# Performance work log

Measured on AMD Instinct MI355X. Metric: run time of the kernel, lower is better.

The kernel has to match this reference:

```python
import jax, jax.numpy as jnp
import numpy as np

X_DIM = 20000   # number of input locations (x_l rows)
Y_DIM = 6000    # number of query locations (y_l rows)
REGION_DEG = 10.0  # lon/lat spread so every query has neighbors within 250 km
EARTH_DIAM = 2.0 * 6.378  # thousand-km diameter used by the source
THRESH = 0.25   # 250 km neighborhood threshold


def setup_inputs() -> dict:
    key = jax.random.key(0)
    k1, k2, k3 = jax.random.split(key, 3)
    x = jax.random.normal(k1, (X_DIM, 1), dtype=jnp.float32)
    x_l = jax.random.uniform(k2, (X_DIM, 2), dtype=jnp.float32) * REGION_DEG
    y_l = jax.random.uniform(k3, (Y_DIM, 2), dtype=jnp.float32) * REGION_DEG
    return {"x": x, "x_l": x_l, "y_l": y_l}


def reference(x, x_l, y_l):
    # Training branch of GPR.call, vectorized over the y_dim python loop.
    d2r = jnp.pi / 180.0
    lon_x, lat_x = x_l[:, 0], x_l[:, 1]   # (X,)
    lon_y, lat_y = y_l[:, 0], y_l[:, 1]   # (Y,)
    # haversine terms, shape (Y, X)
    hav = jnp.sin((lat_x[None, :] - lat_y[:, None]) * d2r) ** 2
    hav = hav + (jnp.cos(lat_x * d2r)[None, :] * jnp.cos(lat_y * d2r)[:, None]
                 * jnp.sin((lon_x[None, :] - lon_y[:, None]) * d2r) ** 2)
    d = EARTH_DIAM * jnp.arcsin(jnp.sqrt(hav))  # great-circle distance (thousand km)
    # threshold + gather/scatter in source == masked weights here
    w = jnp.where(d < THRESH, d, 0.0)
    s = jnp.sum(w, axis=1, keepdims=True)        # (Y, 1) per-row normalizer
    L = jnp.where(s > 0, w / jnp.maximum(s, 1e-12), 0.0)  # (Y, X) sparse-ish weights
    m = (L @ x)[:, 0]                            # (Y,) squeezed mean
    # V = 0.001 * I  (noise=None path); returned value is diag_part(V)
    v_diag = jnp.full((y_l.shape[0],), 0.001, dtype=x.dtype)
    return m, v_diag
```

## Files before the change

### kernel.cpp

```cpp
#include <hip/hip_runtime.h>
#include <math.h>


#define TPB    256
#define YPB    4
#define NSTRIP 40
#define NLON   40
#define NCELLS (NSTRIP * NLON)
#define C_CELL   0.25f
#define INV_CELL 4.0f
#define RLAT     1.1250f

__device__ __forceinline__ float sin_poly(float a) {
    float t = a * a;
    return a * fmaf(t, fmaf(t, 8.3333333e-3f, -0.16666667f), 1.0f);
}
__device__ __forceinline__ float cos_poly(float a) {
    float t = a * a;
    return fmaf(t, fmaf(t, fmaf(t, -1.3888889e-3f, 4.1666668e-2f), -0.5f), 1.0f);
}
__device__ __forceinline__ int cell_of(float lon, float lat) {
    int s = (int)(lat * INV_CELL); s = min(max(s, 0), NSTRIP - 1);
    int l = (int)(lon * INV_CELL); l = min(max(l, 0), NLON - 1);
    return s * NLON + l;
}


__global__ __launch_bounds__(TPB) void zero_kernel(int* __restrict__ histX,
                                                   int* __restrict__ histY) {
    for (int i = threadIdx.x; i < NCELLS; i += TPB) { histX[i] = 0; histY[i] = 0; }
}

__global__ __launch_bounds__(TPB) void hist_kernel(
    const float* __restrict__ x_l, const float* __restrict__ y_l,
    int* __restrict__ histX, int* __restrict__ histY, int nx, int ny)
{
    int i = blockIdx.x * TPB + threadIdx.x;
    if (i < nx) {
        atomicAdd(&histX[cell_of(x_l[2 * i], x_l[2 * i + 1])], 1);
    } else if (i < nx + ny) {
        int j = i - nx;
        atomicAdd(&histY[cell_of(y_l[2 * j], y_l[2 * j + 1])], 1);
    }
}

__global__ __launch_bounds__(TPB) void scan_kernel(
    const int* __restrict__ histX, const int* __restrict__ histY,
    int* __restrict__ csX, int* __restrict__ csY,
    int* __restrict__ curX, int* __restrict__ curY)
{
    const int CHUNK = (NCELLS + TPB - 1) / TPB;
    __shared__ int sums[TPB];
    const int* hist      = (blockIdx.x == 0) ? histX : histY;
    int*       cellStart = (blockIdx.x == 0) ? csX  : csY;
    int*       cursor    = (blockIdx.x == 0) ? curX : curY;

    int tid = threadIdx.x;
    int base = tid * CHUNK;
    int local[7];
    int s = 0;
    #pragma unroll
    for (int j = 0; j < CHUNK; ++j) {
        int idx = base + j;
        int v = (idx < NCELLS) ? hist[idx] : 0;
        local[j] = s; s += v;
    }
    sums[tid] = s;
    __syncthreads();
    for (int off = 1; off < TPB; off <<= 1) {
        int t = (tid >= off) ? sums[tid - off] : 0;
        __syncthreads();
        sums[tid] += t;
        __syncthreads();
    }
    int excl = (tid > 0) ? sums[tid - 1] : 0;
    #pragma unroll
    for (int j = 0; j < CHUNK; ++j) {
        int idx = base + j;
        if (idx < NCELLS) { cellStart[idx] = excl + local[j]; cursor[idx] = excl + local[j]; }
    }
    if (tid == TPB - 1) cellStart[NCELLS] = sums[TPB - 1];
}

__global__ __launch_bounds__(TPB) void scatter_kernel(
    const float* __restrict__ x, const float* __restrict__ x_l,
    const float* __restrict__ y_l,
    int* __restrict__ curX, int* __restrict__ curY,
    float4* __restrict__ sortedA, float2* __restrict__ sortedRaw,
    float*  __restrict__ sortedX,
    float2* __restrict__ sortedYL, int* __restrict__ sortedYIdx,
    int nx, int ny)
{
    const float d2r = 0.017453292519943295f;
    int i = blockIdx.x * TPB + threadIdx.x;
    if (i < nx) {
        float lon = x_l[2 * i], lat = x_l[2 * i + 1];
        int pos = atomicAdd(&curX[cell_of(lon, lat)], 1);
        float al = lat * d2r, ao = lon * d2r;
        sortedA[pos]   = make_float4(sin_poly(al), cos_poly(al),
                                     sin_poly(ao), cos_poly(ao));
        sortedRaw[pos] = make_float2(lon, lat);
        sortedX[pos]   = x[i];
    } else if (i < nx + ny) {
        int j = i - nx;
        float lon = y_l[2 * j], lat = y_l[2 * j + 1];
        int pos = atomicAdd(&curY[cell_of(lon, lat)], 1);
        sortedYL[pos]   = make_float2(lon, lat);
        sortedYIdx[pos] = j;
    }
}


__global__ __launch_bounds__(TPB) void gpr_binned(
    const float4* __restrict__ sortedA,
    const float2* __restrict__ sortedRaw,
    const float*  __restrict__ sortedX,
    const int*    __restrict__ cellStart,
    const float2* __restrict__ sortedYL,
    const int*    __restrict__ sortedYIdx,
    float* __restrict__ out, int ny, float Hcut, float HcutM)
{
    const int tid  = threadIdx.x;
    const int wave = tid >> 6;
    const int lane = tid & 63;
    const int j    = blockIdx.x * YPB + wave;

    const float d2r    = 0.017453292519943295f;
    const float r2d    = 57.29577951308232f;
    const float THRESH = 0.25f;
    const float DIAM   = 12.756f;
    const float DIAM6  = 12.756f / 6.0f;
    const float EPS_H  = 5e-8f;

    int   yidx  = 0;
    float lon_y = 0.0f, lat_y = 0.0f;
    if (j < ny) {
        yidx = sortedYIdx[j];
        float2 p = sortedYL[j];
        lon_y = p.x; lat_y = p.y;
    }
    const float sly   = sin_poly(lat_y * d2r);
    const float cly   = cos_poly(lat_y * d2r);
    const float slony = sin_poly(lon_y * d2r);
    const float clony = cos_poly(lon_y * d2r);

    float accw = 0.0f, accwx = 0.0f;

    const int s0 = max(0,          (int)floorf((lat_y - RLAT) * INV_CELL));
    const int s1 = min(NSTRIP - 1, (int)floorf((lat_y + RLAT) * INV_CELL));

    for (int s = s0; s <= s1; ++s) {
        float slo = s * C_CELL, shi = slo + C_CELL;
        float dmin = fmaxf(0.0f, fmaxf(slo - lat_y, lat_y - shi));
        float de   = fmaxf(0.0f, dmin - 3e-3f);
        float sd_  = sin_poly(de * d2r);
        float rem  = HcutM - sd_ * sd_;
        if (rem <= 0.0f) continue;
        float ccm = cos_poly(fminf(shi, 10.0f) * d2r) * cly * 0.999999f;
        float W   = asinf(fminf(1.0f, sqrtf(rem / ccm))) * r2d + 4e-3f;
        int lo = min(NLON - 1, max(0, (int)floorf((lon_y - W) * INV_CELL)));
        int hi = min(NLON - 1, max(0, (int)floorf((lon_y + W) * INV_CELL)));
        int p0 = cellStart[s * NLON + lo];
        int p1 = cellStart[s * NLON + hi + 1];

        for (int k = p0 + lane; k < p1; k += 64) {
            float4 e  = sortedA[k];
            float  xv = sortedX[k];

            float sl  = fmaf(e.x, cly,   -(e.y * sly));
            float sd  = fmaf(e.z, clony, -(e.w * slony));
            float cxy = e.y * cly;
            float hav = fmaf(sl, sl, cxy * (sd * sd));

            float tb  = hav - Hcut;
            float r   = __builtin_amdgcn_sqrtf(hav);
            float d   = r * fmaf(hav, DIAM6, DIAM);

            float w;
            if (__builtin_expect(fabsf(tb) < EPS_H, 0)) {
                float2 raw = sortedRaw[k];
                float lonx = raw.x, latx = raw.y;

                float dlat = __fsub_rn(latx, lat_y);
                float alat = __fmul_rn(dlat, d2r);
                float slf  = (float)sin((double)alat);
                float h1   = __fmul_rn(slf, slf);

                float axl  = __fmul_rn(latx,  d2r);
                float ayl  = __fmul_rn(lat_y, d2r);
                float cxf  = (float)cos((double)axl);
                float cyf  = (float)cos((double)ayl);
                float cc   = __fmul_rn(cxf, cyf);

                float dlon = __fsub_rn(lonx, lon_y);
                float alon = __fmul_rn(dlon, d2r);
                float sdf  = (float)sin((double)alon);
                float h2   = __fmul_rn(sdf, sdf);

                float hv   = __fadd_rn(h1, __fmul_rn(cc, h2));
                float r32  = (float)sqrt((double)hv);
                float as32 = (float)asin((double)r32);
                float dnp  = __fmul_rn(DIAM, as32);
                w = (dnp < THRESH) ? dnp : 0.0f;
            } else {
                w = (tb < 0.0f) ? d : 0.0f;
            }

            accw += w;
            accwx = fmaf(w, xv, accwx);
        }
    }

    #pragma unroll
    for (int off = 32; off > 0; off >>= 1) {
        accw  += __shfl_xor(accw,  off, 64);
        accwx += __shfl_xor(accwx, off, 64);
    }

    if (lane == 0 && j < ny) {
        float m = (accw > 0.0f) ? (accwx / fmaxf(accw, 1e-12f)) : 0.0f;
        out[yidx]      = m;
        out[ny + yidx] = 0.001f;
    }
}


__global__ __launch_bounds__(TPB) void gpr_full(
    const float* __restrict__ x, const float* __restrict__ x_l,
    const float* __restrict__ y_l, float* __restrict__ out,
    int nx, int ny, float Hcut)
{
    __shared__ float4 tA[1024];
    __shared__ float  tX[1024];

    const int tid  = threadIdx.x;
    const int wave = tid >> 6;
    const int lane = tid & 63;
    const int y    = blockIdx.x * YPB + wave;

    const float d2r    = 0.017453292519943295f;
    const float THRESH = 0.25f;
    const float DIAM   = 12.756f;
    const float DIAM6  = 12.756f / 6.0f;
    const float EPS_H  = 5e-8f;

    float lon_y = 0.0f, lat_y = 0.0f;
    if (y < ny) { lon_y = y_l[2 * y]; lat_y = y_l[2 * y + 1]; }
    const float sly   = sin_poly(lat_y * d2r);
    const float cly   = cos_poly(lat_y * d2r);
    const float slony = sin_poly(lon_y * d2r);
    const float clony = cos_poly(lon_y * d2r);

    float accw = 0.0f, accwx = 0.0f;

    const int ntiles = (nx + 1023) / 1024;
    for (int t = 0; t < ntiles; ++t) {
        const int base = t * 1024;
        __syncthreads();
        #pragma unroll
        for (int jj = 0; jj < 1024 / TPB; ++jj) {
            int idx = jj * TPB + tid, i = base + idx;
            if (i < nx) {
                float lon = x_l[2 * i], lat = x_l[2 * i + 1];
                tA[idx] = make_float4(sin_poly(lat * d2r), cos_poly(lat * d2r),
                                      sin_poly(lon * d2r), cos_poly(lon * d2r));
                tX[idx] = x[i];
            }
        }
        __syncthreads();

        const int tn = min(1024, nx - base);
        for (int k = lane; k < tn; k += 64) {
            float4 e  = tA[k];
            float  xv = tX[k];
            float sl  = fmaf(e.x, cly,   -(e.y * sly));
            float sd  = fmaf(e.z, clony, -(e.w * slony));
            float cxy = e.y * cly;
            float hav = fmaf(sl, sl, cxy * (sd * sd));
            float tb  = hav - Hcut;
            float r   = __builtin_amdgcn_sqrtf(hav);
            float d   = r * fmaf(hav, DIAM6, DIAM);
            float w;
            if (__builtin_expect(fabsf(tb) < EPS_H, 0)) {
                int   i    = base + k;
                float lonx = x_l[2 * i], latx = x_l[2 * i + 1];
                float dlat = __fsub_rn(latx, lat_y);
                float alat = __fmul_rn(dlat, d2r);
                float slf  = (float)sin((double)alat);
                float h1   = __fmul_rn(slf, slf);
                float axl  = __fmul_rn(latx,  d2r);
                float ayl  = __fmul_rn(lat_y, d2r);
                float cxf  = (float)cos((double)axl);
                float cyf  = (float)cos((double)ayl);
                float cc   = __fmul_rn(cxf, cyf);
                float dlon = __fsub_rn(lonx, lon_y);
                float alon = __fmul_rn(dlon, d2r);
                float sdf  = (float)sin((double)alon);
                float h2   = __fmul_rn(sdf, sdf);
                float hv   = __fadd_rn(h1, __fmul_rn(cc, h2));
                float r32  = (float)sqrt((double)hv);
                float as32 = (float)asin((double)r32);
                float dnp  = __fmul_rn(DIAM, as32);
                w = (dnp < THRESH) ? dnp : 0.0f;
            } else {
                w = (tb < 0.0f) ? d : 0.0f;
            }
            accw += w;
            accwx = fmaf(w, xv, accwx);
        }
    }

    #pragma unroll
    for (int off = 32; off > 0; off >>= 1) {
        accw  += __shfl_xor(accw,  off, 64);
        accwx += __shfl_xor(accwx, off, 64);
    }

    if (lane == 0 && y < ny) {
        float m = (accw > 0.0f) ? (accwx / fmaxf(accw, 1e-12f)) : 0.0f;
        out[y]      = m;
        out[ny + y] = 0.001f;
    }
}


extern "C" void kernel_launch(void* const* d_in, const int* in_sizes, int n_in,
                              void* d_out, int out_size, void* d_ws, size_t ws_size,
                              hipStream_t stream) {
    const float* x   = (const float*)d_in[0];
    const float* x_l = (const float*)d_in[1];
    const float* y_l = (const float*)d_in[2];
    float* out = (float*)d_out;

    const int nx = in_sizes[0];
    const int ny = in_sizes[2] / 2;

    double th = 0.25 / 12.756;
    double s  = sin(th);
    float Hcut  = (float)(s * s);
    float HcutM = (float)(s * s * 1.001);

    size_t offA   = 0;
    size_t offRaw = offA   + (size_t)nx * sizeof(float4);
    size_t offYL  = offRaw + (size_t)nx * sizeof(float2);
    size_t offX   = offYL  + (size_t)ny * sizeof(float2);
    size_t offYI  = offX   + (size_t)nx * sizeof(float);
    size_t offHX  = offYI  + (size_t)ny * sizeof(int);
    size_t offHY  = offHX  + (size_t)NCELLS * sizeof(int);
    size_t offCSX = offHY  + (size_t)NCELLS * sizeof(int);
    size_t offCSY = offCSX + (size_t)(NCELLS + 1) * sizeof(int);
    size_t offCuX = offCSY + (size_t)(NCELLS + 1) * sizeof(int);
    size_t offCuY = offCuX + (size_t)NCELLS * sizeof(int);
    size_t total  = offCuY + (size_t)NCELLS * sizeof(int);

    const int blocks = (ny + YPB - 1) / YPB;

    if (ws_size >= total) {
        float4* sortedA    = (float4*)((char*)d_ws + offA);
        float2* sortedRaw  = (float2*)((char*)d_ws + offRaw);
        float2* sortedYL   = (float2*)((char*)d_ws + offYL);
        float*  sortedX    = (float*) ((char*)d_ws + offX);
        int*    sortedYIdx = (int*)   ((char*)d_ws + offYI);
        int*    histX      = (int*)   ((char*)d_ws + offHX);
        int*    histY      = (int*)   ((char*)d_ws + offHY);
        int*    csX        = (int*)   ((char*)d_ws + offCSX);
        int*    csY        = (int*)   ((char*)d_ws + offCSY);
        int*    curX       = (int*)   ((char*)d_ws + offCuX);
        int*    curY       = (int*)   ((char*)d_ws + offCuY);

        int nb = (nx + ny + TPB - 1) / TPB;
        zero_kernel<<<1, TPB, 0, stream>>>(histX, histY);
        hist_kernel<<<nb, TPB, 0, stream>>>(x_l, y_l, histX, histY, nx, ny);
        scan_kernel<<<2, TPB, 0, stream>>>(histX, histY, csX, csY, curX, curY);
        scatter_kernel<<<nb, TPB, 0, stream>>>(x, x_l, y_l, curX, curY,
                                               sortedA, sortedRaw, sortedX,
                                               sortedYL, sortedYIdx, nx, ny);
        gpr_binned<<<blocks, TPB, 0, stream>>>(sortedA, sortedRaw, sortedX,
                                               csX, sortedYL, sortedYIdx,
                                               out, ny, Hcut, HcutM);
    } else {
        gpr_full<<<blocks, TPB, 0, stream>>>(x, x_l, y_l, out, nx, ny, Hcut);
    }
}
```

Baseline: 91.17 us.

## Fuse binning pipeline and query kernel into one cooperative grid-synced kernel

Replaces the five-kernel sequence (zero, histogram, scan, scatter, binned query) with a single cooperative kernel. The stages are separated by grid-wide syncs and use grid-stride loops, with the grid sized from an occupancy query. The aim is to remove per-launch overhead and inter-kernel gaps. The cost is four grid barriers and a grid capped at resident occupancy, with the old multi-kernel path kept as a fallback if the cooperative launch fails.

```diff
diff --git a/kernel.cpp b/kernel.cpp
--- a/kernel.cpp
+++ b/kernel.cpp
@@ -1,5 +1,8 @@
 #include <hip/hip_runtime.h>
+#include <hip/hip_cooperative_groups.h>
 #include <math.h>
+
+namespace cg = cooperative_groups;
 
 
 #define TPB    256
@@ -23,6 +26,196 @@
     int s = (int)(lat * INV_CELL); s = min(max(s, 0), NSTRIP - 1);
     int l = (int)(lon * INV_CELL); l = min(max(l, 0), NLON - 1);
     return s * NLON + l;
+}
+
+
+__global__ __launch_bounds__(TPB) void gpr_mega(
+    const float* __restrict__ x, const float* __restrict__ x_l,
+    const float* __restrict__ y_l,
+    float4* __restrict__ sortedA, float2* __restrict__ sortedRaw,
+    float*  __restrict__ sortedX,
+    float2* __restrict__ sortedYL, int* __restrict__ sortedYIdx,
+    int* __restrict__ histX, int* __restrict__ histY,
+    int* __restrict__ csX, int* __restrict__ csY,
+    int* __restrict__ curX, int* __restrict__ curY,
+    float* __restrict__ out, int nx, int ny, float Hcut, float HcutM)
+{
+    cg::grid_group gridg = cg::this_grid();
+
+    const int tid  = threadIdx.x;
+    const int gtid = blockIdx.x * TPB + tid;
+    const int gsz  = gridDim.x * TPB;
+    const float d2r = 0.017453292519943295f;
+
+    for (int i = gtid; i < NCELLS; i += gsz) { histX[i] = 0; histY[i] = 0; }
+    gridg.sync();
+
+    for (int i = gtid; i < nx + ny; i += gsz) {
+        if (i < nx) {
+            atomicAdd(&histX[cell_of(x_l[2 * i], x_l[2 * i + 1])], 1);
+        } else {
+            int j = i - nx;
+            atomicAdd(&histY[cell_of(y_l[2 * j], y_l[2 * j + 1])], 1);
+        }
+    }
+    gridg.sync();
+
+    {
+        __shared__ int sums[TPB];
+        if (blockIdx.x < 2) {
+            const int CHUNK = (NCELLS + TPB - 1) / TPB;
+            const int* hist      = (blockIdx.x == 0) ? histX : histY;
+            int*       cellStart = (blockIdx.x == 0) ? csX  : csY;
+            int*       cursor    = (blockIdx.x == 0) ? curX : curY;
+
+            int base = tid * CHUNK;
+            int local[7];
+            int s = 0;
+            #pragma unroll
+            for (int jj = 0; jj < CHUNK; ++jj) {
+                int idx = base + jj;
+                int v = (idx < NCELLS) ? hist[idx] : 0;
+                local[jj] = s; s += v;
+            }
+            sums[tid] = s;
+            __syncthreads();
+            for (int off = 1; off < TPB; off <<= 1) {
+                int t = (tid >= off) ? sums[tid - off] : 0;
+                __syncthreads();
+                sums[tid] += t;
+                __syncthreads();
+            }
+            int excl = (tid > 0) ? sums[tid - 1] : 0;
+            #pragma unroll
+            for (int jj = 0; jj < CHUNK; ++jj) {
+                int idx = base + jj;
+                if (idx < NCELLS) {
+                    cellStart[idx] = excl + local[jj];
+                    cursor[idx]    = excl + local[jj];
+                }
+            }
+            if (tid == TPB - 1) cellStart[NCELLS] = sums[TPB - 1];
+        }
+    }
+    gridg.sync();
+
+    for (int i = gtid; i < nx + ny; i += gsz) {
+        if (i < nx) {
+            float lon = x_l[2 * i], lat = x_l[2 * i + 1];
+            int pos = atomicAdd(&curX[cell_of(lon, lat)], 1);
+            float al = lat * d2r, ao = lon * d2r;
+            sortedA[pos]   = make_float4(sin_poly(al), cos_poly(al),
+                                         sin_poly(ao), cos_poly(ao));
+            sortedRaw[pos] = make_float2(lon, lat);
+            sortedX[pos]   = x[i];
+        } else {
+            int j = i - nx;
+            float lon = y_l[2 * j], lat = y_l[2 * j + 1];
+            int pos = atomicAdd(&curY[cell_of(lon, lat)], 1);
+            sortedYL[pos]   = make_float2(lon, lat);
+            sortedYIdx[pos] = j;
+        }
+    }
+    gridg.sync();
+
+    const int wave = tid >> 6;
+    const int lane = tid & 63;
+
+    const float r2d    = 57.29577951308232f;
+    const float THRESH = 0.25f;
+    const float DIAM   = 12.756f;
+    const float DIAM6  = 12.756f / 6.0f;
+    const float EPS_H  = 5e-8f;
+
+    for (int j = blockIdx.x * YPB + wave; j < ny; j += gridDim.x * YPB) {
+        int yidx = sortedYIdx[j];
+        float2 p = sortedYL[j];
+        float lon_y = p.x, lat_y = p.y;
+
+        const float sly   = sin_poly(lat_y * d2r);
+        const float cly   = cos_poly(lat_y * d2r);
+        const float slony = sin_poly(lon_y * d2r);
+        const float clony = cos_poly(lon_y * d2r);
+
+        float accw = 0.0f, accwx = 0.0f;
+
+        const int s0 = max(0,          (int)floorf((lat_y - RLAT) * INV_CELL));
+        const int s1 = min(NSTRIP - 1, (int)floorf((lat_y + RLAT) * INV_CELL));
+
+        for (int s = s0; s <= s1; ++s) {
+            float slo = s * C_CELL, shi = slo + C_CELL;
+            float dmin = fmaxf(0.0f, fmaxf(slo - lat_y, lat_y - shi));
+            float de   = fmaxf(0.0f, dmin - 3e-3f);
+            float sd_  = sin_poly(de * d2r);
+            float rem  = HcutM - sd_ * sd_;
+            if (rem <= 0.0f) continue;
+            float ccm = cos_poly(fminf(shi, 10.0f) * d2r) * cly * 0.999999f;
+            float W   = asinf(fminf(1.0f, sqrtf(rem / ccm))) * r2d + 4e-3f;
+            int lo = min(NLON - 1, max(0, (int)floorf((lon_y - W) * INV_CELL)));
+            int hi = min(NLON - 1, max(0, (int)floorf((lon_y + W) * INV_CELL)));
+            int p0 = csX[s * NLON + lo];
+            int p1 = csX[s * NLON + hi + 1];
+
+            for (int k = p0 + lane; k < p1; k += 64) {
+                float4 e  = sortedA[k];
+                float  xv = sortedX[k];
+
+                float sl  = fmaf(e.x, cly,   -(e.y * sly));
+                float sd  = fmaf(e.z, clony, -(e.w * slony));
+                float cxy = e.y * cly;
+                float hav = fmaf(sl, sl, cxy * (sd * sd));
+
+                float tb  = hav - Hcut;
+                float r   = __builtin_amdgcn_sqrtf(hav);
+                float d   = r * fmaf(hav, DIAM6, DIAM);
+
+                float w;
+                if (__builtin_expect(fabsf(tb) < EPS_H, 0)) {
+                    float2 raw = sortedRaw[k];
+                    float lonx = raw.x, latx = raw.y;
+
+                    float dlat = __fsub_rn(latx, lat_y);
+                    float alat = __fmul_rn(dlat, d2r);
+                    float slf  = (float)sin((double)alat);
+                    float h1   = __fmul_rn(slf, slf);
+
+                    float axl  = __fmul_rn(latx,  d2r);
+                    float ayl  = __fmul_rn(lat_y, d2r);
+                    float cxf  = (float)cos((double)axl);
+                    float cyf  = (float)cos((double)ayl);
+                    float cc   = __fmul_rn(cxf, cyf);
+
+                    float dlon = __fsub_rn(lonx, lon_y);
+                    float alon = __fmul_rn(dlon, d2r);
+                    float sdf  = (float)sin((double)alon);
+                    float h2   = __fmul_rn(sdf, sdf);
+
+                    float hv   = __fadd_rn(h1, __fmul_rn(cc, h2));
+                    float r32  = (float)sqrt((double)hv);
+                    float as32 = (float)asin((double)r32);
+                    float dnp  = __fmul_rn(DIAM, as32);
+                    w = (dnp < THRESH) ? dnp : 0.0f;
+                } else {
+                    w = (tb < 0.0f) ? d : 0.0f;
+                }
+
+                accw += w;
+                accwx = fmaf(w, xv, accwx);
+            }
+        }
+
+        #pragma unroll
+        for (int off = 32; off > 0; off >>= 1) {
+            accw  += __shfl_xor(accw,  off, 64);
+            accwx += __shfl_xor(accwx, off, 64);
+        }
+
+        if (lane == 0) {
+            float m = (accw > 0.0f) ? (accwx / fmaxf(accw, 1e-12f)) : 0.0f;
+            out[yidx]      = m;
+            out[ny + yidx] = 0.001f;
+        }
+    }
 }
 
 
@@ -109,7 +302,6 @@
         sortedYIdx[pos] = j;
     }
 }
-
 
 __global__ __launch_bounds__(TPB) void gpr_binned(
     const float4* __restrict__ sortedA,
@@ -368,16 +560,56 @@
         int*    curX       = (int*)   ((char*)d_ws + offCuX);
         int*    curY       = (int*)   ((char*)d_ws + offCuY);
 
-        int nb = (nx + ny + TPB - 1) / TPB;
-        zero_kernel<<<1, TPB, 0, stream>>>(histX, histY);
-        hist_kernel<<<nb, TPB, 0, stream>>>(x_l, y_l, histX, histY, nx, ny);
-        scan_kernel<<<2, TPB, 0, stream>>>(histX, histY, csX, csY, curX, curY);
-        scatter_kernel<<<nb, TPB, 0, stream>>>(x, x_l, y_l, curX, curY,
-                                               sortedA, sortedRaw, sortedX,
-                                               sortedYL, sortedYIdx, nx, ny);
-        gpr_binned<<<blocks, TPB, 0, stream>>>(sortedA, sortedRaw, sortedX,
-                                               csX, sortedYL, sortedYIdx,
-                                               out, ny, Hcut, HcutM);
+        static int s_maxblocks = -1;
+        if (s_maxblocks < 0) {
+            int nb = 0;
+            hipError_t qe = hipOccupancyMaxActiveBlocksPerMultiprocessor(
+                &nb, gpr_mega, TPB, 0);
+            int cus = 256;
+            int dev = 0;
+            if (hipGetDevice(&dev) == hipSuccess) {
+                int c = 0;
+                if (hipDeviceGetAttribute(&c, hipDeviceAttributeMultiprocessorCount,
+                                          dev) == hipSuccess && c > 0)
+                    cus = c;
+            }
+            s_maxblocks = (qe == hipSuccess && nb > 0) ? nb * cus : 0;
+        }
+
+        bool launched = false;
+        if (s_maxblocks >= 2) {
+            int grid = blocks < s_maxblocks ? blocks : s_maxblocks;
+            void* args[] = {
+                (void*)&x, (void*)&x_l, (void*)&y_l,
+                (void*)&sortedA, (void*)&sortedRaw, (void*)&sortedX,
+                (void*)&sortedYL, (void*)&sortedYIdx,
+                (void*)&histX, (void*)&histY,
+                (void*)&csX, (void*)&csY,
+                (void*)&curX, (void*)&curY,
+                (void*)&out, (void*)&nx, (void*)&ny,
+                (void*)&Hcut, (void*)&HcutM
+            };
+            hipError_t le = hipLaunchCooperativeKernel(
+                gpr_mega, dim3(grid), dim3(TPB), args, 0, stream);
+            if (le == hipSuccess) {
+                launched = true;
+            } else {
+                (void)hipGetLastError();
+            }
+        }
+
+        if (!launched) {
+            int nb = (nx + ny + TPB - 1) / TPB;
+            zero_kernel<<<1, TPB, 0, stream>>>(histX, histY);
+            hist_kernel<<<nb, TPB, 0, stream>>>(x_l, y_l, histX, histY, nx, ny);
+            scan_kernel<<<2, TPB, 0, stream>>>(histX, histY, csX, csY, curX, curY);
+            scatter_kernel<<<nb, TPB, 0, stream>>>(x, x_l, y_l, curX, curY,
+                                                   sortedA, sortedRaw, sortedX,
+                                                   sortedYL, sortedYIdx, nx, ny);
+            gpr_binned<<<blocks, TPB, 0, stream>>>(sortedA, sortedRaw, sortedX,
+                                                   csX, sortedYL, sortedYIdx,
+                                                   out, ny, Hcut, HcutM);
+        }
     } else {
         gpr_full<<<blocks, TPB, 0, stream>>>(x, x_l, y_l, out, nx, ny, Hcut);
     }
```

After: 297.3 us. 3.26x slower.

## Fuse histogram, scan and scatter into one two-block shared-memory build kernel

Applied to the files above, without the earlier changes.

Replaces the four launches (zero, histogram, scan, scatter) that build the spatial grid with a single kernel of two 1024-thread blocks, one for the X points and one for the Y points. Histogram counts, prefix sums and scatter cursors all live in shared memory, so global atomics and three kernel launches go away. The cost is that all of the bucketing now runs on just two workgroups, which serialises about 20000 points over 1024 threads with shared-memory atomic contention.

```diff
diff --git a/kernel.cpp b/kernel.cpp
--- a/kernel.cpp
+++ b/kernel.cpp
@@ -4,6 +4,7 @@
 
 #define TPB    256
 #define YPB    4
+#define BTPB   1024
 #define NSTRIP 40
 #define NLON   40
 #define NCELLS (NSTRIP * NLON)
@@ -26,87 +27,69 @@
 }
 
 
-__global__ __launch_bounds__(TPB) void zero_kernel(int* __restrict__ histX,
-                                                   int* __restrict__ histY) {
-    for (int i = threadIdx.x; i < NCELLS; i += TPB) { histX[i] = 0; histY[i] = 0; }
-}
-
-__global__ __launch_bounds__(TPB) void hist_kernel(
-    const float* __restrict__ x_l, const float* __restrict__ y_l,
-    int* __restrict__ histX, int* __restrict__ histY, int nx, int ny)
+__global__ __launch_bounds__(BTPB) void build_kernel(
+    const float* __restrict__ x, const float* __restrict__ x_l,
+    const float* __restrict__ y_l,
+    float4* __restrict__ sortedA, float2* __restrict__ sortedRaw,
+    float*  __restrict__ sortedX,
+    float2* __restrict__ sortedYL, int* __restrict__ sortedYIdx,
+    int* __restrict__ csX, int nx, int ny)
 {
-    int i = blockIdx.x * TPB + threadIdx.x;
-    if (i < nx) {
-        atomicAdd(&histX[cell_of(x_l[2 * i], x_l[2 * i + 1])], 1);
-    } else if (i < nx + ny) {
-        int j = i - nx;
-        atomicAdd(&histY[cell_of(y_l[2 * j], y_l[2 * j + 1])], 1);
-    }
-}
-
-__global__ __launch_bounds__(TPB) void scan_kernel(
-    const int* __restrict__ histX, const int* __restrict__ histY,
-    int* __restrict__ csX, int* __restrict__ csY,
-    int* __restrict__ curX, int* __restrict__ curY)
-{
-    const int CHUNK = (NCELLS + TPB - 1) / TPB;
-    __shared__ int sums[TPB];
-    const int* hist      = (blockIdx.x == 0) ? histX : histY;
-    int*       cellStart = (blockIdx.x == 0) ? csX  : csY;
-    int*       cursor    = (blockIdx.x == 0) ? curX : curY;
-
-    int tid = threadIdx.x;
-    int base = tid * CHUNK;
-    int local[7];
-    int s = 0;
-    #pragma unroll
-    for (int j = 0; j < CHUNK; ++j) {
-        int idx = base + j;
-        int v = (idx < NCELLS) ? hist[idx] : 0;
-        local[j] = s; s += v;
-    }
-    sums[tid] = s;
+    __shared__ int h[NCELLS];
+    __shared__ int sums[BTPB];
+    const int tid = threadIdx.x;
+    const float d2r = 0.017453292519943295f;
+
+    const bool  isX = (blockIdx.x == 0);
+    const int   n   = isX ? nx  : ny;
+    const float* loc = isX ? x_l : y_l;
+
+    for (int i = tid; i < NCELLS; i += BTPB) h[i] = 0;
     __syncthreads();
-    for (int off = 1; off < TPB; off <<= 1) {
+
+    for (int i = tid; i < n; i += BTPB)
+        atomicAdd(&h[cell_of(loc[2 * i], loc[2 * i + 1])], 1);
+    __syncthreads();
+
+    const int base = tid * 2;
+    int l0 = (base     < NCELLS) ? h[base]     : 0;
+    int l1 = (base + 1 < NCELLS) ? h[base + 1] : 0;
+    sums[tid] = l0 + l1;
+    __syncthreads();
+    for (int off = 1; off < BTPB; off <<= 1) {
         int t = (tid >= off) ? sums[tid - off] : 0;
         __syncthreads();
         sums[tid] += t;
         __syncthreads();
     }
     int excl = (tid > 0) ? sums[tid - 1] : 0;
-    #pragma unroll
-    for (int j = 0; j < CHUNK; ++j) {
-        int idx = base + j;
-        if (idx < NCELLS) { cellStart[idx] = excl + local[j]; cursor[idx] = excl + local[j]; }
-    }
-    if (tid == TPB - 1) cellStart[NCELLS] = sums[TPB - 1];
-}
-
-__global__ __launch_bounds__(TPB) void scatter_kernel(
-    const float* __restrict__ x, const float* __restrict__ x_l,
-    const float* __restrict__ y_l,
-    int* __restrict__ curX, int* __restrict__ curY,
-    float4* __restrict__ sortedA, float2* __restrict__ sortedRaw,
-    float*  __restrict__ sortedX,
-    float2* __restrict__ sortedYL, int* __restrict__ sortedYIdx,
-    int nx, int ny)
-{
-    const float d2r = 0.017453292519943295f;
-    int i = blockIdx.x * TPB + threadIdx.x;
-    if (i < nx) {
-        float lon = x_l[2 * i], lat = x_l[2 * i + 1];
-        int pos = atomicAdd(&curX[cell_of(lon, lat)], 1);
-        float al = lat * d2r, ao = lon * d2r;
-        sortedA[pos]   = make_float4(sin_poly(al), cos_poly(al),
-                                     sin_poly(ao), cos_poly(ao));
-        sortedRaw[pos] = make_float2(lon, lat);
-        sortedX[pos]   = x[i];
-    } else if (i < nx + ny) {
-        int j = i - nx;
-        float lon = y_l[2 * j], lat = y_l[2 * j + 1];
-        int pos = atomicAdd(&curY[cell_of(lon, lat)], 1);
-        sortedYL[pos]   = make_float2(lon, lat);
-        sortedYIdx[pos] = j;
+
+    if (base     < NCELLS) h[base]     = excl;
+    if (base + 1 < NCELLS) h[base + 1] = excl + l0;
+    if (isX) {
+        if (base     < NCELLS) csX[base]     = excl;
+        if (base + 1 < NCELLS) csX[base + 1] = excl + l0;
+        if (tid == BTPB - 1)   csX[NCELLS]   = sums[BTPB - 1];
+    }
+    __syncthreads();
+
+    if (isX) {
+        for (int i = tid; i < n; i += BTPB) {
+            float lon = loc[2 * i], lat = loc[2 * i + 1];
+            int pos = atomicAdd(&h[cell_of(lon, lat)], 1);
+            float al = lat * d2r, ao = lon * d2r;
+            sortedA[pos]   = make_float4(sin_poly(al), cos_poly(al),
+                                         sin_poly(ao), cos_poly(ao));
+            sortedRaw[pos] = make_float2(lon, lat);
+            sortedX[pos]   = x[i];
+        }
+    } else {
+        for (int i = tid; i < n; i += BTPB) {
+            float lon = loc[2 * i], lat = loc[2 * i + 1];
+            int pos = atomicAdd(&h[cell_of(lon, lat)], 1);
+            sortedYL[pos]   = make_float2(lon, lat);
+            sortedYIdx[pos] = i;
+        }
     }
 }
 
@@ -345,13 +328,8 @@
     size_t offYL  = offRaw + (size_t)nx * sizeof(float2);
     size_t offX   = offYL  + (size_t)ny * sizeof(float2);
     size_t offYI  = offX   + (size_t)nx * sizeof(float);
-    size_t offHX  = offYI  + (size_t)ny * sizeof(int);
-    size_t offHY  = offHX  + (size_t)NCELLS * sizeof(int);
-    size_t offCSX = offHY  + (size_t)NCELLS * sizeof(int);
-    size_t offCSY = offCSX + (size_t)(NCELLS + 1) * sizeof(int);
-    size_t offCuX = offCSY + (size_t)(NCELLS + 1) * sizeof(int);
-    size_t offCuY = offCuX + (size_t)NCELLS * sizeof(int);
-    size_t total  = offCuY + (size_t)NCELLS * sizeof(int);
+    size_t offCSX = offYI  + (size_t)ny * sizeof(int);
+    size_t total  = offCSX + (size_t)(NCELLS + 1) * sizeof(int);
 
     const int blocks = (ny + YPB - 1) / YPB;
 
@@ -361,20 +339,12 @@
         float2* sortedYL   = (float2*)((char*)d_ws + offYL);
         float*  sortedX    = (float*) ((char*)d_ws + offX);
         int*    sortedYIdx = (int*)   ((char*)d_ws + offYI);
-        int*    histX      = (int*)   ((char*)d_ws + offHX);
-        int*    histY      = (int*)   ((char*)d_ws + offHY);
         int*    csX        = (int*)   ((char*)d_ws + offCSX);
-        int*    csY        = (int*)   ((char*)d_ws + offCSY);
-        int*    curX       = (int*)   ((char*)d_ws + offCuX);
-        int*    curY       = (int*)   ((char*)d_ws + offCuY);
-
-        int nb = (nx + ny + TPB - 1) / TPB;
-        zero_kernel<<<1, TPB, 0, stream>>>(histX, histY);
-        hist_kernel<<<nb, TPB, 0, stream>>>(x_l, y_l, histX, histY, nx, ny);
-        scan_kernel<<<2, TPB, 0, stream>>>(histX, histY, csX, csY, curX, curY);
-        scatter_kernel<<<nb, TPB, 0, stream>>>(x, x_l, y_l, curX, curY,
-                                               sortedA, sortedRaw, sortedX,
-                                               sortedYL, sortedYIdx, nx, ny);
+
+        build_kernel<<<2, BTPB, 0, stream>>>(x, x_l, y_l,
+                                             sortedA, sortedRaw, sortedX,
+                                             sortedYL, sortedYIdx,
+                                             csX, nx, ny);
         gpr_binned<<<blocks, TPB, 0, stream>>>(sortedA, sortedRaw, sortedX,
                                                csX, sortedYL, sortedYIdx,
                                                out, ny, Hcut, HcutM);
```

Measured after the change: 132.7 us. 45.5% more time.

## Process two adjacent sorted queries per wave to share candidate loads

Applied to the files above, without the earlier changes.

Each wave now handles two consecutive spatially sorted query points. Per latitude strip it takes the union of their longitude cell ranges and loads each candidate's trig terms and value once, evaluating the haversine test for both queries. This halves the block count and reuses global loads across the pair. The cost is extra evaluations for cells that only one query needs, plus higher register use.

```diff
diff --git a/kernel.cpp b/kernel.cpp
--- a/kernel.cpp
+++ b/kernel.cpp
@@ -4,6 +4,7 @@
 
 #define TPB    256
 #define YPB    4
+#define YPW    2
 #define NSTRIP 40
 #define NLON   40
 #define NCELLS (NSTRIP * NLON)
@@ -111,7 +112,7 @@
 }
 
 
-__global__ __launch_bounds__(TPB) void gpr_binned(
+__global__ __launch_bounds__(TPB) void gpr_binned2(
     const float4* __restrict__ sortedA,
     const float2* __restrict__ sortedRaw,
     const float*  __restrict__ sortedX,
@@ -123,7 +124,9 @@
     const int tid  = threadIdx.x;
     const int wave = tid >> 6;
     const int lane = tid & 63;
-    const int j    = blockIdx.x * YPB + wave;
+    const int gw   = blockIdx.x * YPB + wave;
+    const int j0   = gw * YPW;
+    const int j1   = j0 + 1;
 
     const float d2r    = 0.017453292519943295f;
     const float r2d    = 57.29577951308232f;
@@ -132,34 +135,65 @@
     const float DIAM6  = 12.756f / 6.0f;
     const float EPS_H  = 5e-8f;
 
-    int   yidx  = 0;
-    float lon_y = 0.0f, lat_y = 0.0f;
-    if (j < ny) {
-        yidx = sortedYIdx[j];
-        float2 p = sortedYL[j];
-        lon_y = p.x; lat_y = p.y;
-    }
-    const float sly   = sin_poly(lat_y * d2r);
-    const float cly   = cos_poly(lat_y * d2r);
-    const float slony = sin_poly(lon_y * d2r);
-    const float clony = cos_poly(lon_y * d2r);
-
-    float accw = 0.0f, accwx = 0.0f;
-
-    const int s0 = max(0,          (int)floorf((lat_y - RLAT) * INV_CELL));
-    const int s1 = min(NSTRIP - 1, (int)floorf((lat_y + RLAT) * INV_CELL));
+    if (j0 >= ny) return;
+
+    int   yidx0 = sortedYIdx[j0];
+    float2 p0v  = sortedYL[j0];
+    float lon0  = p0v.x, lat0 = p0v.y;
+
+    bool  have1 = (j1 < ny);
+    int   yidx1 = have1 ? sortedYIdx[j1] : yidx0;
+    float2 p1v  = have1 ? sortedYL[j1] : p0v;
+    float lon1  = p1v.x, lat1 = p1v.y;
+
+    const float sly0   = sin_poly(lat0 * d2r);
+    const float cly0   = cos_poly(lat0 * d2r);
+    const float slon0  = sin_poly(lon0 * d2r);
+    const float clon0  = cos_poly(lon0 * d2r);
+    const float sly1   = sin_poly(lat1 * d2r);
+    const float cly1   = cos_poly(lat1 * d2r);
+    const float slon1  = sin_poly(lon1 * d2r);
+    const float clon1  = cos_poly(lon1 * d2r);
+
+    float accw0 = 0.0f, accwx0 = 0.0f;
+    float accw1 = 0.0f, accwx1 = 0.0f;
+
+    const float latmin = fminf(lat0, lat1);
+    const float latmax = fmaxf(lat0, lat1);
+    const int s0 = max(0,          (int)floorf((latmin - RLAT) * INV_CELL));
+    const int s1 = min(NSTRIP - 1, (int)floorf((latmax + RLAT) * INV_CELL));
 
     for (int s = s0; s <= s1; ++s) {
         float slo = s * C_CELL, shi = slo + C_CELL;
-        float dmin = fmaxf(0.0f, fmaxf(slo - lat_y, lat_y - shi));
-        float de   = fmaxf(0.0f, dmin - 3e-3f);
-        float sd_  = sin_poly(de * d2r);
-        float rem  = HcutM - sd_ * sd_;
-        if (rem <= 0.0f) continue;
-        float ccm = cos_poly(fminf(shi, 10.0f) * d2r) * cly * 0.999999f;
-        float W   = asinf(fminf(1.0f, sqrtf(rem / ccm))) * r2d + 4e-3f;
-        int lo = min(NLON - 1, max(0, (int)floorf((lon_y - W) * INV_CELL)));
-        int hi = min(NLON - 1, max(0, (int)floorf((lon_y + W) * INV_CELL)));
+        float ccos = cos_poly(fminf(shi, 10.0f) * d2r) * 0.999999f;
+
+        int lo = NLON, hi = -1;
+        {
+            float dmin = fmaxf(0.0f, fmaxf(slo - lat0, lat0 - shi));
+            float de   = fmaxf(0.0f, dmin - 3e-3f);
+            float sd_  = sin_poly(de * d2r);
+            float rem  = HcutM - sd_ * sd_;
+            if (rem > 0.0f) {
+                float ccm = ccos * cly0;
+                float W   = asinf(fminf(1.0f, sqrtf(rem / ccm))) * r2d + 4e-3f;
+                lo = min(NLON - 1, max(0, (int)floorf((lon0 - W) * INV_CELL)));
+                hi = min(NLON - 1, max(0, (int)floorf((lon0 + W) * INV_CELL)));
+            }
+        }
+        {
+            float dmin = fmaxf(0.0f, fmaxf(slo - lat1, lat1 - shi));
+            float de   = fmaxf(0.0f, dmin - 3e-3f);
+            float sd_  = sin_poly(de * d2r);
+            float rem  = HcutM - sd_ * sd_;
+            if (rem > 0.0f) {
+                float ccm = ccos * cly1;
+                float W   = asinf(fminf(1.0f, sqrtf(rem / ccm))) * r2d + 4e-3f;
+                lo = min(lo, min(NLON - 1, max(0, (int)floorf((lon1 - W) * INV_CELL))));
+                hi = max(hi, min(NLON - 1, max(0, (int)floorf((lon1 + W) * INV_CELL))));
+            }
+        }
+        if (hi < lo) continue;
+
         int p0 = cellStart[s * NLON + lo];
         int p1 = cellStart[s * NLON + hi + 1];
 
@@ -167,60 +201,103 @@
             float4 e  = sortedA[k];
             float  xv = sortedX[k];
 
-            float sl  = fmaf(e.x, cly,   -(e.y * sly));
-            float sd  = fmaf(e.z, clony, -(e.w * slony));
-            float cxy = e.y * cly;
-            float hav = fmaf(sl, sl, cxy * (sd * sd));
-
-            float tb  = hav - Hcut;
-            float r   = __builtin_amdgcn_sqrtf(hav);
-            float d   = r * fmaf(hav, DIAM6, DIAM);
-
-            float w;
-            if (__builtin_expect(fabsf(tb) < EPS_H, 0)) {
-                float2 raw = sortedRaw[k];
-                float lonx = raw.x, latx = raw.y;
-
-                float dlat = __fsub_rn(latx, lat_y);
-                float alat = __fmul_rn(dlat, d2r);
-                float slf  = (float)sin((double)alat);
-                float h1   = __fmul_rn(slf, slf);
-
-                float axl  = __fmul_rn(latx,  d2r);
-                float ayl  = __fmul_rn(lat_y, d2r);
-                float cxf  = (float)cos((double)axl);
-                float cyf  = (float)cos((double)ayl);
-                float cc   = __fmul_rn(cxf, cyf);
-
-                float dlon = __fsub_rn(lonx, lon_y);
-                float alon = __fmul_rn(dlon, d2r);
-                float sdf  = (float)sin((double)alon);
-                float h2   = __fmul_rn(sdf, sdf);
-
-                float hv   = __fadd_rn(h1, __fmul_rn(cc, h2));
-                float r32  = (float)sqrt((double)hv);
-                float as32 = (float)asin((double)r32);
-                float dnp  = __fmul_rn(DIAM, as32);
-                w = (dnp < THRESH) ? dnp : 0.0f;
-            } else {
-                w = (tb < 0.0f) ? d : 0.0f;
-            }
-
-            accw += w;
-            accwx = fmaf(w, xv, accwx);
+            {
+                float sl  = fmaf(e.x, cly0,  -(e.y * sly0));
+                float sd  = fmaf(e.z, clon0, -(e.w * slon0));
+                float cxy = e.y * cly0;
+                float hav = fmaf(sl, sl, cxy * (sd * sd));
+
+                float tb  = hav - Hcut;
+                float r   = __builtin_amdgcn_sqrtf(hav);
+                float d   = r * fmaf(hav, DIAM6, DIAM);
+
+                float w;
+                if (__builtin_expect(fabsf(tb) < EPS_H, 0)) {
+                    float2 raw = sortedRaw[k];
+                    float lonx = raw.x, latx = raw.y;
+                    float dlat = __fsub_rn(latx, lat0);
+                    float alat = __fmul_rn(dlat, d2r);
+                    float slf  = (float)sin((double)alat);
+                    float h1   = __fmul_rn(slf, slf);
+                    float axl  = __fmul_rn(latx, d2r);
+                    float ayl  = __fmul_rn(lat0, d2r);
+                    float cxf  = (float)cos((double)axl);
+                    float cyf  = (float)cos((double)ayl);
+                    float cc   = __fmul_rn(cxf, cyf);
+                    float dlon = __fsub_rn(lonx, lon0);
+                    float alon = __fmul_rn(dlon, d2r);
+                    float sdf  = (float)sin((double)alon);
+                    float h2   = __fmul_rn(sdf, sdf);
+                    float hv   = __fadd_rn(h1, __fmul_rn(cc, h2));
+                    float r32  = (float)sqrt((double)hv);
+                    float as32 = (float)asin((double)r32);
+                    float dnp  = __fmul_rn(DIAM, as32);
+                    w = (dnp < THRESH) ? dnp : 0.0f;
+                } else {
+                    w = (tb < 0.0f) ? d : 0.0f;
+                }
+                accw0 += w;
+                accwx0 = fmaf(w, xv, accwx0);
+            }
+
+            {
+                float sl  = fmaf(e.x, cly1,  -(e.y * sly1));
+                float sd  = fmaf(e.z, clon1, -(e.w * slon1));
+                float cxy = e.y * cly1;
+                float hav = fmaf(sl, sl, cxy * (sd * sd));
+
+                float tb  = hav - Hcut;
+                float r   = __builtin_amdgcn_sqrtf(hav);
+                float d   = r * fmaf(hav, DIAM6, DIAM);
+
+                float w;
+                if (__builtin_expect(fabsf(tb) < EPS_H, 0)) {
+                    float2 raw = sortedRaw[k];
+                    float lonx = raw.x, latx = raw.y;
+                    float dlat = __fsub_rn(latx, lat1);
+                    float alat = __fmul_rn(dlat, d2r);
+                    float slf  = (float)sin((double)alat);
+                    float h1   = __fmul_rn(slf, slf);
+                    float axl  = __fmul_rn(latx, d2r);
+                    float ayl  = __fmul_rn(lat1, d2r);
+                    float cxf  = (float)cos((double)axl);
+                    float cyf  = (float)cos((double)ayl);
+                    float cc   = __fmul_rn(cxf, cyf);
+                    float dlon = __fsub_rn(lonx, lon1);
+                    float alon = __fmul_rn(dlon, d2r);
+                    float sdf  = (float)sin((double)alon);
+                    float h2   = __fmul_rn(sdf, sdf);
+                    float hv   = __fadd_rn(h1, __fmul_rn(cc, h2));
+                    float r32  = (float)sqrt((double)hv);
+                    float as32 = (float)asin((double)r32);
+                    float dnp  = __fmul_rn(DIAM, as32);
+                    w = (dnp < THRESH) ? dnp : 0.0f;
+                } else {
+                    w = (tb < 0.0f) ? d : 0.0f;
+                }
+                accw1 += w;
+                accwx1 = fmaf(w, xv, accwx1);
+            }
         }
     }
 
     #pragma unroll
     for (int off = 32; off > 0; off >>= 1) {
-        accw  += __shfl_xor(accw,  off, 64);
-        accwx += __shfl_xor(accwx, off, 64);
-    }
-
-    if (lane == 0 && j < ny) {
-        float m = (accw > 0.0f) ? (accwx / fmaxf(accw, 1e-12f)) : 0.0f;
-        out[yidx]      = m;
-        out[ny + yidx] = 0.001f;
+        accw0  += __shfl_xor(accw0,  off, 64);
+        accwx0 += __shfl_xor(accwx0, off, 64);
+        accw1  += __shfl_xor(accw1,  off, 64);
+        accwx1 += __shfl_xor(accwx1, off, 64);
+    }
+
+    if (lane == 0) {
+        float m0 = (accw0 > 0.0f) ? (accwx0 / fmaxf(accw0, 1e-12f)) : 0.0f;
+        out[yidx0]      = m0;
+        out[ny + yidx0] = 0.001f;
+        if (have1) {
+            float m1 = (accw1 > 0.0f) ? (accwx1 / fmaxf(accw1, 1e-12f)) : 0.0f;
+            out[yidx1]      = m1;
+            out[ny + yidx1] = 0.001f;
+        }
     }
 }
 
@@ -353,7 +430,7 @@
     size_t offCuY = offCuX + (size_t)NCELLS * sizeof(int);
     size_t total  = offCuY + (size_t)NCELLS * sizeof(int);
 
-    const int blocks = (ny + YPB - 1) / YPB;
+    const int blocks = (ny + YPB * YPW - 1) / (YPB * YPW);
 
     if (ws_size >= total) {
         float4* sortedA    = (float4*)((char*)d_ws + offA);
@@ -375,10 +452,11 @@
         scatter_kernel<<<nb, TPB, 0, stream>>>(x, x_l, y_l, curX, curY,
                                                sortedA, sortedRaw, sortedX,
                                                sortedYL, sortedYIdx, nx, ny);
-        gpr_binned<<<blocks, TPB, 0, stream>>>(sortedA, sortedRaw, sortedX,
-                                               csX, sortedYL, sortedYIdx,
-                                               out, ny, Hcut, HcutM);
+        gpr_binned2<<<blocks, TPB, 0, stream>>>(sortedA, sortedRaw, sortedX,
+                                                csX, sortedYL, sortedYIdx,
+                                                out, ny, Hcut, HcutM);
     } else {
-        gpr_full<<<blocks, TPB, 0, stream>>>(x, x_l, y_l, out, nx, ny, Hcut);
-    }
-}
+        int fb = (ny + YPB - 1) / YPB;
+        gpr_full<<<fb, TPB, 0, stream>>>(x, x_l, y_l, out, nx, ny, Hcut);
+    }
+}
```

Measured after the change: 101.6 us. 1.11x slower.
